# Kernel optimization log

Hardware: AMD Instinct MI355X
Metric: run time of the kernel (lower is better)

## Reference

```python
import jax, jax.numpy as jnp
import numpy as np

N_NODES = 50000
N_EDGES = 800000
IN_DIM = 768
HIDDEN = 256
N_CLASSES = 10
N_GRAPHS = 128


def setup_inputs() -> dict:
    key = jax.random.key(0)
    ks = jax.random.split(key, 10)
    emb = jax.random.normal(ks[0], (N_NODES, IN_DIM), dtype=jnp.float32)
    edge_index = jax.random.randint(ks[1], (2, N_EDGES), 0, N_NODES, dtype=jnp.int32)
    batch = jnp.sort(jax.random.randint(ks[2], (N_NODES,), 0, N_GRAPHS, dtype=jnp.int32))
    # GCNConv weights (glorot-ish scale) and biases
    W1 = jax.random.normal(ks[3], (IN_DIM, HIDDEN), dtype=jnp.float32) / np.sqrt(IN_DIM)
    b1 = jnp.zeros((HIDDEN,), dtype=jnp.float32)
    W2 = jax.random.normal(ks[4], (HIDDEN, HIDDEN), dtype=jnp.float32) / np.sqrt(HIDDEN)
    b2 = jnp.zeros((HIDDEN,), dtype=jnp.float32)
    Wfc = jax.random.normal(ks[5], (HIDDEN, N_CLASSES), dtype=jnp.float32) / np.sqrt(HIDDEN)
    bfc = jnp.zeros((N_CLASSES,), dtype=jnp.float32)
    return {"emb": emb, "edge_index": edge_index, "batch": batch,
            "W1": W1, "b1": b1, "W2": W2, "b2": b2, "Wfc": Wfc, "bfc": bfc}


def _gcn_conv(x, src, dst, W, b, n_nodes):
    # PyG GCNConv: x' = D^{-1/2} (A + I) D^{-1/2} X W + b, self-loops included
    h = x @ W                                   # [N, H] dense GEMM
    deg = jax.ops.segment_sum(jnp.ones_like(dst, dtype=h.dtype), dst,
                              num_segments=n_nodes)
    dinv = jnp.where(deg > 0, jax.lax.rsqrt(deg), 0.0)
    norm = dinv[src] * dinv[dst]                # [E+N]
    msgs = h[src] * norm[:, None]               # gather [E+N, H]
    out = jax.ops.segment_sum(msgs, dst, num_segments=n_nodes)  # scatter-add
    return out + b


def reference(emb, edge_index, batch, W1, b1, W2, b2, Wfc, bfc):
    n_nodes = emb.shape[0]
    loops = jnp.arange(n_nodes, dtype=edge_index.dtype)
    src = jnp.concatenate([edge_index[0], loops])  # add self-loops
    dst = jnp.concatenate([edge_index[1], loops])

    x = jax.nn.relu(_gcn_conv(emb, src, dst, W1, b1, n_nodes))
    # F.dropout(p=0.3) is a no-op in eval mode (training=False)
    x = _gcn_conv(x, src, dst, W2, b2, n_nodes)

    # global_mean_pool over graph ids
    sums = jax.ops.segment_sum(x, batch, num_segments=N_GRAPHS)
    cnts = jax.ops.segment_sum(jnp.ones((n_nodes,), dtype=x.dtype), batch,
                               num_segments=N_GRAPHS)
    pooled = sums / jnp.maximum(cnts, 1.0)[:, None]  # [G, H]
    return pooled @ Wfc + bfc                        # [G, C]
```

## Files before the change

### kernel.cpp

```cpp
#include <hip/hip_runtime.h>

#define N_NODES 50000
#define N_EDGES 800000
#define IN_DIM 768
#define HIDDEN 256
#define N_CLASSES 10
#define N_GRAPHS 128
#define KSPLIT 256
#define GTILE 32
#define KCHUNK ((N_NODES + KSPLIT - 1) / KSPLIT)

typedef __attribute__((ext_vector_type(8))) short bf16x8;
typedef __attribute__((ext_vector_type(4))) float f32x4;
typedef __attribute__((ext_vector_type(8))) unsigned short u16x8;

__device__ __forceinline__ float bf2f(unsigned short u) {
    union { unsigned int i; float f; } c; c.i = ((unsigned int)u) << 16; return c.f;
}
__device__ __forceinline__ unsigned short f2bf(float f) {
    unsigned int x = __float_as_uint(f);
    return (unsigned short)((x + 0x7fffu + ((x >> 16) & 1u)) >> 16);
}

__device__ __forceinline__ void gload16(const void* g, void* l) {
    __builtin_amdgcn_global_load_lds((const __attribute__((address_space(1))) void*)g,
                                     (__attribute__((address_space(3))) void*)l, 16, 0, 0);
}

__global__ void zero_int(int* p, int n) {
    int i = blockIdx.x * blockDim.x + threadIdx.x;
    if (i < n) p[i] = 0;
}

__global__ void zero_f32(float* p, int n) {
    int i = blockIdx.x * blockDim.x + threadIdx.x;
    if (i < n) p[i] = 0.f;
}

__global__ void hist_dst(const int* __restrict__ dst, int* __restrict__ cnt) {
    int e = blockIdx.x * blockDim.x + threadIdx.x;
    if (e < N_EDGES) atomicAdd(&cnt[dst[e]], 1);
}

__global__ __launch_bounds__(1024) void scan_kernel(const int* __restrict__ cnt,
                                                    int* __restrict__ rowstart,
                                                    int* __restrict__ cursor,
                                                    float* __restrict__ dinv) {
    __shared__ int wsum[16];
    __shared__ int chunk_carry;
    const int tid = threadIdx.x, lane = tid & 63, wid = tid >> 6;
    if (tid == 0) chunk_carry = 0;
    __syncthreads();
    for (int base = 0; base < N_NODES; base += 1024) {
        int i = base + tid;
        int v = (i < N_NODES) ? cnt[i] : 0;
        if (i < N_NODES) dinv[i] = rsqrtf(1.0f + (float)v);
        int s = v;
#pragma unroll
        for (int d = 1; d < 64; d <<= 1) { int t = __shfl_up(s, d); if (lane >= d) s += t; }
        if (lane == 63) wsum[wid] = s;
        __syncthreads();
        if (tid < 16) {
            int ww = wsum[tid];
#pragma unroll
            for (int d = 1; d < 16; d <<= 1) { int t = __shfl_up(ww, d); if (tid >= d) ww += t; }
            wsum[tid] = ww;
        }
        __syncthreads();
        int wpre = (wid == 0) ? 0 : wsum[wid - 1];
        int excl = chunk_carry + wpre + s - v;
        if (i < N_NODES) { rowstart[i] = excl; cursor[i] = excl; }
        int total = wsum[15];
        __syncthreads();
        if (tid == 0) chunk_carry += total;
        __syncthreads();
    }
    if (threadIdx.x == 0) rowstart[N_NODES] = chunk_carry;
}

__global__ void scatter_edges(const int* __restrict__ src, const int* __restrict__ dst,
                              const int* __restrict__ batch, const float* __restrict__ dinv,
                              int* __restrict__ cursor, int* __restrict__ col,
                              float* __restrict__ nrm, float* __restrict__ S) {
    int e = blockIdx.x * blockDim.x + threadIdx.x;
    if (e >= N_EDGES) return;
    int s = src[e], d = dst[e];
    int pos = atomicAdd(&cursor[d], 1);
    float w = dinv[s] * dinv[d];
    col[pos] = s;
    nrm[pos] = w;
    atomicAdd(&S[(size_t)s * 128 + batch[d]], w);
}

__global__ void add_self_S(const int* __restrict__ batch, const float* __restrict__ dinv,
                           float* __restrict__ S) {
    int n = blockIdx.x * blockDim.x + threadIdx.x;
    if (n >= N_NODES) return;
    float w = dinv[n]; w *= w;
    S[(size_t)n * 128 + batch[n]] += w;
}

__global__ __launch_bounds__(256) void transpose_w_bf16(const float* __restrict__ W,
                                                        unsigned short* __restrict__ WT, int K) {
    __shared__ float t[32][33];
    int tx = threadIdx.x & 31, ty = threadIdx.x >> 5;
    int k0 = blockIdx.x * 32, n0 = blockIdx.y * 32;
#pragma unroll
    for (int i = 0; i < 4; ++i) {
        int k = k0 + ty + i * 8;
        t[ty + i * 8][tx] = W[(size_t)k * 256 + n0 + tx];
    }
    __syncthreads();
#pragma unroll
    for (int i = 0; i < 4; ++i) {
        int n = n0 + ty + i * 8;
        WT[(size_t)n * K + k0 + tx] = f2bf(t[tx][ty + i * 8]);
    }
}

template <int K, bool CVT>
__global__ __launch_bounds__(256, 2) void gemm_mfma(const void* __restrict__ Av,
                                                    const unsigned short* __restrict__ BT,
                                                    unsigned short* __restrict__ C, int M) {
    constexpr int NS = K / 64;
    __shared__ uint4 sm[5120];
    uint4* As = sm;
    uint4* Bs = sm + 1024;
    const int tid = threadIdx.x;
    const int lane = tid & 63, w = tid >> 6;
    const int lr = lane & 15, kg = lane >> 4;
    const int bm = blockIdx.x * 64;

    const int ra = tid >> 2;
    const int ca = (tid & 3) * 2;
    int rga = bm + ra; rga = rga < M ? rga : M - 1;

    f32x4 acc[16] = {};

    {
        if constexpr (CVT) {
            const float* p = &((const float*)Av)[(size_t)rga * K + ca * 8];
            float4 u0 = ((const float4*)p)[0], u1 = ((const float4*)p)[1];
            float4 u2 = ((const float4*)p)[2], u3 = ((const float4*)p)[3];
            u16x8 o0, o1;
            o0[0] = f2bf(u0.x); o0[1] = f2bf(u0.y); o0[2] = f2bf(u0.z); o0[3] = f2bf(u0.w);
            o0[4] = f2bf(u1.x); o0[5] = f2bf(u1.y); o0[6] = f2bf(u1.z); o0[7] = f2bf(u1.w);
            o1[0] = f2bf(u2.x); o1[1] = f2bf(u2.y); o1[2] = f2bf(u2.z); o1[3] = f2bf(u2.w);
            o1[4] = f2bf(u3.x); o1[5] = f2bf(u3.y); o1[6] = f2bf(u3.z); o1[7] = f2bf(u3.w);
            *(u16x8*)&As[ra * 8 + (ca ^ (ra & 7))] = o0;
            *(u16x8*)&As[ra * 8 + ((ca + 1) ^ (ra & 7))] = o1;
        } else {
            const unsigned short* Ab = (const unsigned short*)Av;
            uint4 v0 = *(const uint4*)&Ab[(size_t)rga * K + ca * 8];
            uint4 v1 = *(const uint4*)&Ab[(size_t)rga * K + ca * 8 + 8];
            As[ra * 8 + (ca ^ (ra & 7))] = v0;
            As[ra * 8 + ((ca + 1) ^ (ra & 7))] = v1;
        }
#pragma unroll
        for (int i = 0; i < 8; ++i) {
            int glin = w * 512 + i * 64 + lane;
            int n = glin >> 3, g = glin & 7;
            int gs = g ^ (n & 7);
            gload16(&BT[(size_t)n * K + gs * 8], &Bs[w * 512 + i * 64]);
        }
    }
    __syncthreads();

    for (int k = 0; k < NS; ++k) {
        const int cur = k & 1, nxt = cur ^ 1;
        const int kk1 = (k + 1) * 64;
        float4 u0, u1, u2, u3;
        uint4 v0, v1;
        if (k + 1 < NS) {
#pragma unroll
            for (int i = 0; i < 8; ++i) {
                int glin = w * 512 + i * 64 + lane;
                int n = glin >> 3, g = glin & 7;
                int gs = g ^ (n & 7);
                gload16(&BT[(size_t)n * K + kk1 + gs * 8], &Bs[nxt * 2048 + w * 512 + i * 64]);
            }
            if constexpr (CVT) {
                const float* p = &((const float*)Av)[(size_t)rga * K + kk1 + ca * 8];
                u0 = ((const float4*)p)[0]; u1 = ((const float4*)p)[1];
                u2 = ((const float4*)p)[2]; u3 = ((const float4*)p)[3];
            } else {
                const unsigned short* Ab = (const unsigned short*)Av;
                v0 = *(const uint4*)&Ab[(size_t)rga * K + kk1 + ca * 8];
                v1 = *(const uint4*)&Ab[(size_t)rga * K + kk1 + ca * 8 + 8];
            }
        }
#pragma unroll
        for (int h = 0; h < 2; ++h) {
            int r0 = 16 * w + lr;
            int gc = 4 * h + kg;
            bf16x8 a0 = *(const bf16x8*)&As[cur * 512 + r0 * 8 + (gc ^ (r0 & 7))];
#pragma unroll
            for (int f = 0; f < 16; ++f) {
                int nr = 16 * f + lr;
                bf16x8 bf = *(const bf16x8*)&Bs[cur * 2048 + nr * 8 + (gc ^ (nr & 7))];
                acc[f] = __builtin_amdgcn_mfma_f32_16x16x32_bf16(bf, a0, acc[f], 0, 0, 0);
            }
        }
        if (k + 1 < NS) {
            if constexpr (CVT) {
                u16x8 o0, o1;
                o0[0] = f2bf(u0.x); o0[1] = f2bf(u0.y); o0[2] = f2bf(u0.z); o0[3] = f2bf(u0.w);
                o0[4] = f2bf(u1.x); o0[5] = f2bf(u1.y); o0[6] = f2bf(u1.z); o0[7] = f2bf(u1.w);
                o1[0] = f2bf(u2.x); o1[1] = f2bf(u2.y); o1[2] = f2bf(u2.z); o1[3] = f2bf(u2.w);
                o1[4] = f2bf(u3.x); o1[5] = f2bf(u3.y); o1[6] = f2bf(u3.z); o1[7] = f2bf(u3.w);
                *(u16x8*)&As[nxt * 512 + ra * 8 + (ca ^ (ra & 7))] = o0;
                *(u16x8*)&As[nxt * 512 + ra * 8 + ((ca + 1) ^ (ra & 7))] = o1;
            } else {
                As[nxt * 512 + ra * 8 + (ca ^ (ra & 7))] = v0;
                As[nxt * 512 + ra * 8 + ((ca + 1) ^ (ra & 7))] = v1;
            }
        }
        __syncthreads();
    }

    int orow = bm + 16 * w + lr;
    if (orow < M) {
#pragma unroll
        for (int f = 0; f < 16; ++f) {
            ushort4 o = make_ushort4(f2bf(acc[f][0]), f2bf(acc[f][1]),
                                     f2bf(acc[f][2]), f2bf(acc[f][3]));
            *(ushort4*)&C[(size_t)orow * 256 + 16 * f + 4 * kg] = o;
        }
    }
}

template <bool RELU, bool OUTBF>
__global__ __launch_bounds__(256) void agg_csr(const unsigned short* __restrict__ h,
                                               const float* __restrict__ dinv,
                                               const int* __restrict__ rowstart,
                                               const int* __restrict__ col,
                                               const float* __restrict__ nrm,
                                               const float* __restrict__ bias,
                                               void* __restrict__ outv) {
    int node = (blockIdx.x * 256 + threadIdx.x) >> 6;
    if (node >= N_NODES) return;
    const int lane = threadIdx.x & 63;
    const int half = lane >> 5, sl = lane & 31;

    float dd = dinv[node];
    float acc[8] = {};

    {
        u16x8 hv = *(const u16x8*)&h[(size_t)node * 256 + sl * 8];
        float wgt = half ? 0.f : dd * dd;
#pragma unroll
        for (int i = 0; i < 8; ++i) acc[i] += bf2f(hv[i]) * wgt;
    }

    int j0 = rowstart[node], jend = rowstart[node + 1];
    int j = j0;
    for (; j + 8 <= jend; j += 8) {
        int s0 = col[j + half];
        int s1 = col[j + 2 + half];
        int s2 = col[j + 4 + half];
        int s3 = col[j + 6 + half];
        float n0 = nrm[j + half], n1 = nrm[j + 2 + half];
        float n2 = nrm[j + 4 + half], n3 = nrm[j + 6 + half];
        u16x8 v0 = *(const u16x8*)&h[(size_t)s0 * 256 + sl * 8];
        u16x8 v1 = *(const u16x8*)&h[(size_t)s1 * 256 + sl * 8];
        u16x8 v2 = *(const u16x8*)&h[(size_t)s2 * 256 + sl * 8];
        u16x8 v3 = *(const u16x8*)&h[(size_t)s3 * 256 + sl * 8];
#pragma unroll
        for (int i = 0; i < 8; ++i)
            acc[i] += bf2f(v0[i]) * n0 + bf2f(v1[i]) * n1 + bf2f(v2[i]) * n2 + bf2f(v3[i]) * n3;
    }
    for (; j < jend; j += 2) {
        int sidx = j + half;
        bool p = sidx < jend;
        int si = p ? sidx : (jend - 1);
        int s = col[si];
        float w = p ? nrm[si] : 0.f;
        u16x8 v = *(const u16x8*)&h[(size_t)s * 256 + sl * 8];
#pragma unroll
        for (int i = 0; i < 8; ++i) acc[i] += bf2f(v[i]) * w;
    }

#pragma unroll
    for (int i = 0; i < 8; ++i) acc[i] += __shfl_xor(acc[i], 32);

    if (half == 0) {
        float4 b0 = *(const float4*)&bias[sl * 8];
        float4 b1 = *(const float4*)&bias[sl * 8 + 4];
        acc[0] += b0.x; acc[1] += b0.y; acc[2] += b0.z; acc[3] += b0.w;
        acc[4] += b1.x; acc[5] += b1.y; acc[6] += b1.z; acc[7] += b1.w;
        if (RELU) {
#pragma unroll
            for (int i = 0; i < 8; ++i) acc[i] = fmaxf(acc[i], 0.f);
        }
        if (OUTBF) {
            u16x8 o;
#pragma unroll
            for (int i = 0; i < 8; ++i) o[i] = f2bf(acc[i]);
            *(u16x8*)((unsigned short*)outv + (size_t)node * 256 + sl * 8) = o;
        } else {
            float* ob = (float*)outv + (size_t)node * 256 + sl * 8;
            *(float4*)ob = make_float4(acc[0], acc[1], acc[2], acc[3]);
            *(float4*)(ob + 4) = make_float4(acc[4], acc[5], acc[6], acc[7]);
        }
    }
}

__global__ __launch_bounds__(256) void pool_gemm(const unsigned short* __restrict__ x1,
                                                 const float* __restrict__ S,
                                                 float* __restrict__ Ppart) {
    const int t = threadIdx.x;
    const int cg = t & 31;
    const int gq = t >> 5;
    const int ks = blockIdx.x;
    const int g0 = blockIdx.y * GTILE + gq * 4;
    int s0 = ks * KCHUNK;
    int s1 = s0 + KCHUNK; if (s1 > N_NODES) s1 = N_NODES;

    float acc[4][8] = {};

    int srow = s0;
    for (; srow + 2 <= s1; srow += 2) {
        u16x8 xv0 = *(const u16x8*)&x1[(size_t)srow * 256 + cg * 8];
        u16x8 xv1 = *(const u16x8*)&x1[(size_t)(srow + 1) * 256 + cg * 8];
        float4 sv0 = *(const float4*)&S[(size_t)srow * 128 + g0];
        float4 sv1 = *(const float4*)&S[(size_t)(srow + 1) * 128 + g0];
        float xf0[8], xf1[8];
#pragma unroll
        for (int ch = 0; ch < 8; ++ch) { xf0[ch] = bf2f(xv0[ch]); xf1[ch] = bf2f(xv1[ch]); }
#pragma unroll
        for (int ch = 0; ch < 8; ++ch) {
            acc[0][ch] += xf0[ch] * sv0.x + xf1[ch] * sv1.x;
            acc[1][ch] += xf0[ch] * sv0.y + xf1[ch] * sv1.y;
            acc[2][ch] += xf0[ch] * sv0.z + xf1[ch] * sv1.z;
            acc[3][ch] += xf0[ch] * sv0.w + xf1[ch] * sv1.w;
        }
    }
    if (srow < s1) {
        u16x8 xv = *(const u16x8*)&x1[(size_t)srow * 256 + cg * 8];
        float4 sv = *(const float4*)&S[(size_t)srow * 128 + g0];
        float xf[8];
#pragma unroll
        for (int ch = 0; ch < 8; ++ch) xf[ch] = bf2f(xv[ch]);
#pragma unroll
        for (int ch = 0; ch < 8; ++ch) {
            acc[0][ch] += xf[ch] * sv.x;
            acc[1][ch] += xf[ch] * sv.y;
            acc[2][ch] += xf[ch] * sv.z;
            acc[3][ch] += xf[ch] * sv.w;
        }
    }
#pragma unroll
    for (int g = 0; g < 4; ++g) {
        float* dstp = &Ppart[((size_t)ks * N_GRAPHS + g0 + g) * 256 + cg * 8];
        *(float4*)dstp = make_float4(acc[g][0], acc[g][1], acc[g][2], acc[g][3]);
        *(float4*)(dstp + 4) = make_float4(acc[g][4], acc[g][5], acc[g][6], acc[g][7]);
    }
}

__global__ __launch_bounds__(256) void reduce_P(const float* __restrict__ Ppart,
                                                float* __restrict__ P) {
    int idx = blockIdx.x * 256 + threadIdx.x;
    float s = 0.f;
    for (int b = 0; b < KSPLIT; ++b) s += Ppart[(size_t)b * (N_GRAPHS * 256) + idx];
    P[idx] = s;
}

__global__ __launch_bounds__(256) void head(const float* __restrict__ P,
                                            const int* __restrict__ batch,
                                            const float* __restrict__ W2,
                                            const float* __restrict__ b2,
                                            const float* __restrict__ Wfc,
                                            const float* __restrict__ bfc,
                                            float* __restrict__ out) {
    int g = blockIdx.x;
    int c = threadIdx.x;
    int lo = 0, hi = N_NODES;
    while (lo < hi) { int m = (lo + hi) >> 1; if (batch[m] < g) lo = m + 1; else hi = m; }
    int lo2 = lo, hi2 = N_NODES;
    while (lo2 < hi2) { int m = (lo2 + hi2) >> 1; if (batch[m] < g + 1) lo2 = m + 1; else hi2 = m; }
    float inv = 1.0f / fmaxf((float)(lo2 - lo), 1.0f);

    __shared__ float pp[256];
    __shared__ float zz[256];
    pp[c] = P[(size_t)g * 256 + c] * inv;
    __syncthreads();
    float z = b2[c];
    for (int k = 0; k < 256; ++k) z += pp[k] * W2[(size_t)k * 256 + c];
    zz[c] = z;
    __syncthreads();
    if (c < N_CLASSES) {
        float o = bfc[c];
        for (int k = 0; k < 256; ++k) o += zz[k] * Wfc[k * N_CLASSES + c];
        out[g * N_CLASSES + c] = o;
    }
}

extern "C" void kernel_launch(void* const* d_in, const int* in_sizes, int n_in,
                              void* d_out, int out_size, void* d_ws, size_t ws_size,
                              hipStream_t stream) {
    const float* emb  = (const float*)d_in[0];
    const int*   eidx = (const int*)d_in[1];
    const int*   batch= (const int*)d_in[2];
    const float* W1   = (const float*)d_in[3];
    const float* b1   = (const float*)d_in[4];
    const float* W2   = (const float*)d_in[5];
    const float* b2   = (const float*)d_in[6];
    const float* Wfc  = (const float*)d_in[7];
    const float* bfc  = (const float*)d_in[8];
    float* out = (float*)d_out;

    const int* src = eidx;
    const int* dst = eidx + N_EDGES;

    char* ws = (char*)d_ws;
    size_t off = 0;
    auto alloc = [&](size_t bytes) { void* p = ws + off; off += (bytes + 1023) & ~(size_t)1023; return p; };
    int*   rowcnt   = (int*)alloc(N_NODES * 4);
    int*   rowstart = (int*)alloc((N_NODES + 1) * 4);
    int*   cursor   = (int*)alloc(N_NODES * 4);
    int*   col      = (int*)alloc(N_EDGES * 4);
    float* nrm      = (float*)alloc(N_EDGES * 4);
    float* dinv     = (float*)alloc(N_NODES * 4);
    float* S        = (float*)alloc((size_t)N_NODES * 128 * 4);
    float* Ppart    = (float*)alloc((size_t)KSPLIT * N_GRAPHS * 256 * 4);
    float* P        = (float*)alloc((size_t)N_GRAPHS * 256 * 4);
    unsigned short* W1T = (unsigned short*)alloc((size_t)HIDDEN * IN_DIM * 2);
    unsigned short* bufH = (unsigned short*)alloc((size_t)N_NODES * 256 * 2);
    unsigned short* x1 = (unsigned short*)alloc((size_t)N_NODES * 256 * 2);

    const int NB = (N_NODES + 255) / 256;
    const int EBk = (N_EDGES + 255) / 256;
    const int AGG_B = (N_NODES * 64 + 255) / 256;
    dim3 gemm_grid((N_NODES + 63) / 64, 1);

    zero_int<<<NB, 256, 0, stream>>>(rowcnt, N_NODES);
    hist_dst<<<EBk, 256, 0, stream>>>(dst, rowcnt);
    scan_kernel<<<1, 1024, 0, stream>>>(rowcnt, rowstart, cursor, dinv);
    zero_f32<<<(N_NODES * 128 + 255) / 256, 256, 0, stream>>>(S, N_NODES * 128);
    scatter_edges<<<EBk, 256, 0, stream>>>(src, dst, batch, dinv, cursor, col, nrm, S);
    add_self_S<<<NB, 256, 0, stream>>>(batch, dinv, S);

    transpose_w_bf16<<<dim3(IN_DIM / 32, 8), 256, 0, stream>>>(W1, W1T, IN_DIM);

    gemm_mfma<IN_DIM, true><<<gemm_grid, 256, 0, stream>>>(emb, W1T, bufH, N_NODES);
    agg_csr<true, true><<<AGG_B, 256, 0, stream>>>(bufH, dinv, rowstart, col, nrm, b1, x1);

    pool_gemm<<<dim3(KSPLIT, N_GRAPHS / GTILE), 256, 0, stream>>>(x1, S, Ppart);
    reduce_P<<<(N_GRAPHS * 256) / 256, 256, 0, stream>>>(Ppart, P);

    head<<<N_GRAPHS, 256, 0, stream>>>(P, batch, W2, b2, Wfc, bfc, out);
}
```

Baseline: 420.8 us.

## Transpose pooling matrix S to graph-major and build it from CSR order

Stores the node-to-graph aggregation matrix as ST[graph][node] instead of S[node][graph]. It is built in a separate pass over CSR-ordered edges, using the graph id of each edge recorded during the scatter. The pool GEMM now reads four scalar rows of ST per node instead of one float4. The intent is to improve locality of the atomic scatter into S, since CSR order groups edges by destination and so by graph, but it adds an extra kernel, a gid array, and scalar strided loads in pool_gemm.

Result: slower. 440.5 us (+4.7%).

```diff
diff --git a/kernel.cpp b/kernel.cpp
--- a/kernel.cpp
+++ b/kernel.cpp
@@ -81,23 +81,29 @@
 __global__ void scatter_edges(const int* __restrict__ src, const int* __restrict__ dst,
                               const int* __restrict__ batch, const float* __restrict__ dinv,
                               int* __restrict__ cursor, int* __restrict__ col,
-                              float* __restrict__ nrm, float* __restrict__ S) {
+                              float* __restrict__ nrm, int* __restrict__ gid) {
     int e = blockIdx.x * blockDim.x + threadIdx.x;
     if (e >= N_EDGES) return;
     int s = src[e], d = dst[e];
     int pos = atomicAdd(&cursor[d], 1);
-    float w = dinv[s] * dinv[d];
     col[pos] = s;
-    nrm[pos] = w;
-    atomicAdd(&S[(size_t)s * 128 + batch[d]], w);
-}
-
-__global__ void add_self_S(const int* __restrict__ batch, const float* __restrict__ dinv,
-                           float* __restrict__ S) {
+    nrm[pos] = dinv[s] * dinv[d];
+    gid[pos] = batch[d];
+}
+
+__global__ void build_ST(const int* __restrict__ col, const float* __restrict__ nrm,
+                         const int* __restrict__ gid, float* __restrict__ ST) {
+    int j = blockIdx.x * blockDim.x + threadIdx.x;
+    if (j >= N_EDGES) return;
+    atomicAdd(&ST[(size_t)gid[j] * N_NODES + col[j]], nrm[j]);
+}
+
+__global__ void add_self_ST(const int* __restrict__ batch, const float* __restrict__ dinv,
+                            float* __restrict__ ST) {
     int n = blockIdx.x * blockDim.x + threadIdx.x;
     if (n >= N_NODES) return;
     float w = dinv[n]; w *= w;
-    S[(size_t)n * 128 + batch[n]] += w;
+    ST[(size_t)batch[n] * N_NODES + n] += w;
 }
 
 __global__ __launch_bounds__(256) void transpose_w_bf16(const float* __restrict__ W,
@@ -306,7 +312,7 @@
 }
 
 __global__ __launch_bounds__(256) void pool_gemm(const unsigned short* __restrict__ x1,
-                                                 const float* __restrict__ S,
+                                                 const float* __restrict__ ST,
                                                  float* __restrict__ Ppart) {
     const int t = threadIdx.x;
     const int cg = t & 31;
@@ -316,37 +322,42 @@
     int s0 = ks * KCHUNK;
     int s1 = s0 + KCHUNK; if (s1 > N_NODES) s1 = N_NODES;
 
+    const float* st0 = &ST[(size_t)(g0 + 0) * N_NODES];
+    const float* st1 = &ST[(size_t)(g0 + 1) * N_NODES];
+    const float* st2 = &ST[(size_t)(g0 + 2) * N_NODES];
+    const float* st3 = &ST[(size_t)(g0 + 3) * N_NODES];
+
     float acc[4][8] = {};
 
     int srow = s0;
     for (; srow + 2 <= s1; srow += 2) {
         u16x8 xv0 = *(const u16x8*)&x1[(size_t)srow * 256 + cg * 8];
         u16x8 xv1 = *(const u16x8*)&x1[(size_t)(srow + 1) * 256 + cg * 8];
-        float4 sv0 = *(const float4*)&S[(size_t)srow * 128 + g0];
-        float4 sv1 = *(const float4*)&S[(size_t)(srow + 1) * 128 + g0];
+        float sa0 = st0[srow], sb0 = st1[srow], sc0 = st2[srow], sd0 = st3[srow];
+        float sa1 = st0[srow + 1], sb1 = st1[srow + 1], sc1 = st2[srow + 1], sd1 = st3[srow + 1];
         float xf0[8], xf1[8];
 #pragma unroll
         for (int ch = 0; ch < 8; ++ch) { xf0[ch] = bf2f(xv0[ch]); xf1[ch] = bf2f(xv1[ch]); }
 #pragma unroll
         for (int ch = 0; ch < 8; ++ch) {
-            acc[0][ch] += xf0[ch] * sv0.x + xf1[ch] * sv1.x;
-            acc[1][ch] += xf0[ch] * sv0.y + xf1[ch] * sv1.y;
-            acc[2][ch] += xf0[ch] * sv0.z + xf1[ch] * sv1.z;
-            acc[3][ch] += xf0[ch] * sv0.w + xf1[ch] * sv1.w;
+            acc[0][ch] += xf0[ch] * sa0 + xf1[ch] * sa1;
+            acc[1][ch] += xf0[ch] * sb0 + xf1[ch] * sb1;
+            acc[2][ch] += xf0[ch] * sc0 + xf1[ch] * sc1;
+            acc[3][ch] += xf0[ch] * sd0 + xf1[ch] * sd1;
         }
     }
     if (srow < s1) {
         u16x8 xv = *(const u16x8*)&x1[(size_t)srow * 256 + cg * 8];
-        float4 sv = *(const float4*)&S[(size_t)srow * 128 + g0];
+        float sa = st0[srow], sb = st1[srow], sc = st2[srow], sd = st3[srow];
         float xf[8];
 #pragma unroll
         for (int ch = 0; ch < 8; ++ch) xf[ch] = bf2f(xv[ch]);
 #pragma unroll
         for (int ch = 0; ch < 8; ++ch) {
-            acc[0][ch] += xf[ch] * sv.x;
-            acc[1][ch] += xf[ch] * sv.y;
-            acc[2][ch] += xf[ch] * sv.z;
-            acc[3][ch] += xf[ch] * sv.w;
+            acc[0][ch] += xf[ch] * sa;
+            acc[1][ch] += xf[ch] * sb;
+            acc[2][ch] += xf[ch] * sc;
+            acc[3][ch] += xf[ch] * sd;
         }
     }
 #pragma unroll
@@ -420,8 +431,9 @@
     int*   cursor   = (int*)alloc(N_NODES * 4);
     int*   col      = (int*)alloc(N_EDGES * 4);
     float* nrm      = (float*)alloc(N_EDGES * 4);
+    int*   gid      = (int*)alloc(N_EDGES * 4);
     float* dinv     = (float*)alloc(N_NODES * 4);
-    float* S        = (float*)alloc((size_t)N_NODES * 128 * 4);
+    float* ST       = (float*)alloc((size_t)N_GRAPHS * N_NODES * 4);
     float* Ppart    = (float*)alloc((size_t)KSPLIT * N_GRAPHS * 256 * 4);
     float* P        = (float*)alloc((size_t)N_GRAPHS * 256 * 4);
     unsigned short* W1T = (unsigned short*)alloc((size_t)HIDDEN * IN_DIM * 2);
@@ -436,16 +448,17 @@
     zero_int<<<NB, 256, 0, stream>>>(rowcnt, N_NODES);
     hist_dst<<<EBk, 256, 0, stream>>>(dst, rowcnt);
     scan_kernel<<<1, 1024, 0, stream>>>(rowcnt, rowstart, cursor, dinv);
-    zero_f32<<<(N_NODES * 128 + 255) / 256, 256, 0, stream>>>(S, N_NODES * 128);
-    scatter_edges<<<EBk, 256, 0, stream>>>(src, dst, batch, dinv, cursor, col, nrm, S);
-    add_self_S<<<NB, 256, 0, stream>>>(batch, dinv, S);
+    scatter_edges<<<EBk, 256, 0, stream>>>(src, dst, batch, dinv, cursor, col, nrm, gid);
+    zero_f32<<<(N_GRAPHS * N_NODES + 255) / 256, 256, 0, stream>>>(ST, N_GRAPHS * N_NODES);
+    build_ST<<<EBk, 256, 0, stream>>>(col, nrm, gid, ST);
+    add_self_ST<<<NB, 256, 0, stream>>>(batch, dinv, ST);
 
     transpose_w_bf16<<<dim3(IN_DIM / 32, 8), 256, 0, stream>>>(W1, W1T, IN_DIM);
 
     gemm_mfma<IN_DIM, true><<<gemm_grid, 256, 0, stream>>>(emb, W1T, bufH, N_NODES);
     agg_csr<true, true><<<AGG_B, 256, 0, stream>>>(bufH, dinv, rowstart, col, nrm, b1, x1);
 
-    pool_gemm<<<dim3(KSPLIT, N_GRAPHS / GTILE), 256, 0, stream>>>(x1, S, Ppart);
+    pool_gemm<<<dim3(KSPLIT, N_GRAPHS / GTILE), 256, 0, stream>>>(x1, ST, Ppart);
     reduce_P<<<(N_GRAPHS * 256) / 256, 256, 0, stream>>>(Ppart, P);
 
     head<<<N_GRAPHS, 256, 0, stream>>>(P, batch, W2, b2, Wfc, bfc, out);
```
